# Optimization experiments

Measured on AMD Instinct MI355X. Metric: run time of the kernel, lower is better.

## Reference

```python
import jax, jax.numpy as jnp
import numpy as np

HEADS = 4
DIM_HEAD = 32
DIM = 128
EPS = 1e-5


def layer_norm(x, g, b):
    m = jnp.mean(x, axis=-1, keepdims=True)
    v = jnp.var(x, axis=-1, keepdims=True)
    return (x - m) * jax.lax.rsqrt(v + EPS) * g + b


def setup_inputs() -> dict:
    key = jax.random.key(0)
    ks = jax.random.split(key, 24)
    B, D, Hb, Wb = 1, DIM, 50, 50
    N, h, w = 6, 24, 44
    Q = Hb * Wb
    NK = N * h * w
    inner = HEADS * DIM_HEAD
    s = 0.02
    inp = {
        'q': jax.random.normal(ks[0], (B, D, Hb, Wb), jnp.float32),
        'k': jax.random.normal(ks[1], (B, N, D, h, w), jnp.float32),
        'v': jax.random.normal(ks[2], (B, N, D, h, w), jnp.float32),
        'W_logits': jax.random.uniform(ks[3], (B, Q, NK), jnp.float32),
        'vis': jax.random.randint(ks[4], (B, Q, NK), 0, 2, jnp.int32),
        'skip': jax.random.normal(ks[5], (B, D, Hb, Wb), jnp.float32),
        'qn_g': jnp.ones((D,)), 'qn_b': jnp.zeros((D,)),
        'kn_g': jnp.ones((D,)), 'kn_b': jnp.zeros((D,)),
        'vn_g': jnp.ones((D,)), 'vn_b': jnp.zeros((D,)),
        'wq': s * jax.random.normal(ks[6], (inner, D)), 'bq': jnp.zeros((inner,)),
        'wk': s * jax.random.normal(ks[7], (inner, D)), 'bk': jnp.zeros((inner,)),
        'wv': s * jax.random.normal(ks[8], (inner, D)), 'bv': jnp.zeros((inner,)),
        'wproj': s * jax.random.normal(ks[9], (D, inner)), 'bproj': jnp.zeros((D,)),
        'pre_g': jnp.ones((D,)), 'pre_b': jnp.zeros((D,)),
        'w1': s * jax.random.normal(ks[10], (2 * D, D)), 'b1': jnp.zeros((2 * D,)),
        'w2': s * jax.random.normal(ks[11], (D, 2 * D)), 'b2': jnp.zeros((D,)),
        'post_g': jnp.ones((D,)), 'post_b': jnp.zeros((D,)),
    }
    return inp


def reference(q, k, v, W_logits, vis, skip,
              qn_g, qn_b, kn_g, kn_b, vn_g, vn_b,
              wq, bq, wk, bk, wv, bv, wproj, bproj,
              pre_g, pre_b, w1, b1, w2, b2, post_g, post_b):
    B, D, Hb, Wb = q.shape
    Q = Hb * Wb
    scale = DIM_HEAD ** (-0.5)
    # flatten: q -> [B, Q, D]; k,v [B,N,D,h,w] -> [B, NK, D]
    qf = q.reshape(B, D, Q).transpose(0, 2, 1)
    kf = jnp.transpose(k, (0, 1, 3, 4, 2)).reshape(B, -1, D)
    vf = jnp.transpose(v, (0, 1, 3, 4, 2)).reshape(B, -1, D)
    qf = layer_norm(qf, qn_g, qn_b) @ wq.T + bq
    kf = layer_norm(kf, kn_g, kn_b) @ wk.T + bk
    vf = layer_norm(vf, vn_g, vn_b) @ wv.T + bv
    # split heads -> [B, H, Q/K, dh]
    qh = qf.reshape(B, Q, HEADS, DIM_HEAD).transpose(0, 2, 1, 3)
    kh = kf.reshape(B, -1, HEADS, DIM_HEAD).transpose(0, 2, 1, 3)
    vh = vf.reshape(B, -1, HEADS, DIM_HEAD).transpose(0, 2, 1, 3)
    logits = jnp.einsum('bhqd,bhkd->bhqk', qh, kh) * scale
    neg_inf = jnp.finfo(logits.dtype).min
    logits = jnp.where(vis[:, None] == 0, neg_inf, logits)
    logits = logits * W_logits[:, None]
    attn = jax.nn.softmax(logits, axis=-1)
    out = jnp.einsum('bhqk,bhkd->bhqd', attn, vh)
    out = out.transpose(0, 2, 1, 3).reshape(B, Q, HEADS * DIM_HEAD)
    out = out @ wproj.T + bproj
    z = out.transpose(0, 2, 1).reshape(B, D, Hb, Wb) + skip
    zf = z.reshape(B, D, Q).transpose(0, 2, 1)
    zf = layer_norm(zf, pre_g, pre_b)
    hmid = jax.nn.gelu(zf @ w1.T + b1, approximate=False)
    zf = zf + (hmid @ w2.T + b2)
    zf = layer_norm(zf, post_g, post_b)
    return zf.transpose(0, 2, 1).reshape(B, D, Hb, Wb)
```

## Files before the change

### kernel.cpp

```cpp
#include <hip/hip_runtime.h>
#include <hip/hip_bf16.h>

typedef __attribute__((ext_vector_type(8))) short bf16x8;
typedef __attribute__((ext_vector_type(4))) float f32x4;

#define NQ 2500
#define NKK 6336
#define NHEADS 4
#define DHEAD 32
#define CSC 0.25503482f
#define BIGNEG (-1.0e30f)

#define WS_QP 0
#define WS_KP 640000
#define WS_VT 2262016
#define WS_WB 3884032
#define WS_OP 4146176
#define OSPLIT_F 340000
#define OROW_F 136
#define WS_REQ3 8226176ULL
#define WS_REQ4 9586176ULL
#define WS_REQ6 12306176ULL

#define WQB 0
#define WKB 16384
#define WVB 32768
#define WPROJB 49152
#define W1B 65536
#define W2B 98304

#define NTILES_TOTAL 99
#define TQ 16
#define TK 64
#define QBLOCKS 157
#define MQBLOCKS 313

#define KSTR 136
#define VSTR 72
#define PSTR 72
#define ABSTR 68

__device__ __forceinline__ unsigned short bf16bits(float x) {
  union { __hip_bfloat16 h; unsigned short s; } cv;
  cv.h = __float2bfloat16(x);
  return cv.s;
}

__global__ __launch_bounds__(256) void wconv_kernel(
    const float* __restrict__ wq, const float* __restrict__ wk,
    const float* __restrict__ wv, const float* __restrict__ wproj,
    const float* __restrict__ w1, const float* __restrict__ w2,
    __hip_bfloat16* __restrict__ wb)
{
  int e = (blockIdx.x * 256 + threadIdx.x) * 4;
  const float* src; int off;
  if (e < 16384)      { src = wq;    off = e; }
  else if (e < 32768) { src = wk;    off = e - 16384; }
  else if (e < 49152) { src = wv;    off = e - 32768; }
  else if (e < 65536) { src = wproj; off = e - 49152; }
  else if (e < 98304) { src = w1;    off = e - 65536; }
  else                { src = w2;    off = e - 98304; }
  float4 v = *(const float4*)(src + off);
  ushort4 o4;
  o4.x = bf16bits(v.x); o4.y = bf16bits(v.y); o4.z = bf16bits(v.z); o4.w = bf16bits(v.w);
  *(ushort4*)((unsigned short*)wb + e) = o4;
}

__global__ __launch_bounds__(256) void lnproj_kernel(
    const float* __restrict__ qin, const float* __restrict__ kin, const float* __restrict__ vin,
    const float* __restrict__ qn_g, const float* __restrict__ qn_b,
    const float* __restrict__ kn_g, const float* __restrict__ kn_b,
    const float* __restrict__ vn_g, const float* __restrict__ vn_b,
    const __hip_bfloat16* __restrict__ wball,
    const float* __restrict__ bq, const float* __restrict__ bk, const float* __restrict__ bv,
    __hip_bfloat16* __restrict__ Qp, __hip_bfloat16* __restrict__ Kp,
    __hip_bfloat16* __restrict__ Vt)
{
  __shared__ __hip_bfloat16 lxb[32][136];
  __shared__ float lpart[32][8][2];
  __shared__ float lmr[32][2];
  __shared__ float lgb[128], lbeb[128];

  const int t = threadIdx.x;
  const int bb = blockIdx.x;
  int mode, row0;
  const float *in, *g, *be, *bo;
  const __hip_bfloat16* wb;
  if (bb < 79)       { mode = 0; row0 = bb * 32;         in = qin; g = qn_g; be = qn_b; wb = wball + WQB; bo = bq; }
  else if (bb < 277) { mode = 1; row0 = (bb - 79) * 32;  in = kin; g = kn_g; be = kn_b; wb = wball + WKB; bo = bk; }
  else               { mode = 2; row0 = (bb - 277) * 32; in = vin; g = vn_g; be = vn_b; wb = wball + WVB; bo = bv; }

  if (t < 128) { lgb[t] = g[t]; lbeb[t] = be[t]; }

  const int row = t & 31, seg = t >> 5;
  int grow = row0 + row;
  size_t base, dstr;
  bool rvalid = true;
  if (mode == 0) { rvalid = (grow < NQ); base = (size_t)(rvalid ? grow : NQ - 1); dstr = NQ; }
  else { int n = grow / 1056, rr = grow - n * 1056; base = (size_t)n * 135168 + rr; dstr = 1056; }

  float xr[16];
  float s = 0.f, ss = 0.f;
  #pragma unroll
  for (int i = 0; i < 16; ++i) {
    float x = in[base + (size_t)(seg * 16 + i) * dstr];
    xr[i] = x; s += x; ss += x * x;
  }
  lpart[row][seg][0] = s; lpart[row][seg][1] = ss;
  __syncthreads();
  if (t < 32) {
    float S = 0.f, SS = 0.f;
    #pragma unroll
    for (int j = 0; j < 8; ++j) { S += lpart[t][j][0]; SS += lpart[t][j][1]; }
    float mean = S * (1.f / 128.f);
    float var  = SS * (1.f / 128.f) - mean * mean;
    lmr[t][0] = mean;
    lmr[t][1] = rsqrtf(fmaxf(var, 0.f) + 1e-5f);
  }
  __syncthreads();
  {
    float mean = lmr[row][0], rstd = lmr[row][1];
    #pragma unroll
    for (int i = 0; i < 16; ++i) {
      int d = seg * 16 + i;
      lxb[row][d] = __float2bfloat16((xr[i] - mean) * rstd * lgb[d] + lbeb[d]);
    }
  }
  __syncthreads();

  const int wid = t >> 6, lane = t & 63;
  const int n16 = lane & 15, quad = lane >> 4;
  const int ow = wid * 32;

  f32x4 acc[2][2] = {};
  for (int kt = 0; kt < 4; ++kt) {
    bf16x8 af[2];
    #pragma unroll
    for (int mi = 0; mi < 2; ++mi)
      af[mi] = *(const bf16x8*)&lxb[mi * 16 + n16][kt * 32 + quad * 8];
    #pragma unroll
    for (int ni = 0; ni < 2; ++ni) {
      bf16x8 bw = *(const bf16x8*)(wb + (size_t)(ow + ni * 16 + n16) * 128 + kt * 32 + quad * 8);
      #pragma unroll
      for (int mi = 0; mi < 2; ++mi)
        acc[mi][ni] = __builtin_amdgcn_mfma_f32_16x16x32_bf16(af[mi], bw, acc[mi][ni], 0, 0, 0);
    }
  }

  float bias[2];
  #pragma unroll
  for (int ni = 0; ni < 2; ++ni) bias[ni] = bo[ow + ni * 16 + n16];

  #pragma unroll
  for (int mi = 0; mi < 2; ++mi) {
    int gr0 = row0 + mi * 16 + quad * 4;
    if (mode == 2) {
      #pragma unroll
      for (int ni = 0; ni < 2; ++ni) {
        int o = ow + ni * 16 + n16;
        ushort4 v4;
        v4.x = bf16bits(acc[mi][ni][0] + bias[ni]);
        v4.y = bf16bits(acc[mi][ni][1] + bias[ni]);
        v4.z = bf16bits(acc[mi][ni][2] + bias[ni]);
        v4.w = bf16bits(acc[mi][ni][3] + bias[ni]);
        *(ushort4*)((unsigned short*)Vt + (size_t)o * NKK + gr0) = v4;
      }
    } else {
      #pragma unroll
      for (int rg = 0; rg < 4; ++rg) {
        int gr = gr0 + rg;
        if (mode != 0 || gr < NQ) {
          #pragma unroll
          for (int ni = 0; ni < 2; ++ni) {
            int o = ow + ni * 16 + n16;
            __hip_bfloat16 b16 = __float2bfloat16(acc[mi][ni][rg] + bias[ni]);
            if (mode == 0) Qp[(size_t)gr * 128 + o] = b16;
            else           Kp[(size_t)gr * 128 + o] = b16;
          }
        }
      }
    }
  }
}

__global__ __launch_bounds__(256, 3) void attn_kernel(
    const __hip_bfloat16* __restrict__ Qp,
    const __hip_bfloat16* __restrict__ Kp,
    const __hip_bfloat16* __restrict__ Vt,
    const float* __restrict__ Wl,
    const int* __restrict__ vis,
    float* __restrict__ Opart)
{
  __shared__ alignas(16) __hip_bfloat16 lk[TK * KSTR];
  __shared__ alignas(16) __hip_bfloat16 lv[128 * VSTR];
  __shared__ alignas(16) float sc[TQ * ABSTR];
  __shared__ alignas(16) __hip_bfloat16 lp[NHEADS * TQ * PSTR];

  const int t = threadIdx.x;
  const int lane = t & 63;
  const int h = t >> 6;
  const int n16 = lane & 15;
  const int quad = lane >> 4;
  const int q0 = blockIdx.x * TQ;
  const int split = blockIdx.y;
  const int ksplit = gridDim.y;
  const int tstart = (NTILES_TOTAL * split) / ksplit;
  const int ntiles = (NTILES_TOTAL * (split + 1)) / ksplit - tstart;

  int gqa = q0 + n16; if (gqa >= NQ) gqa = NQ - 1;
  bf16x8 aq = *(const bf16x8*)(Qp + (size_t)gqa * 128 + h * DHEAD + quad * 8);

  const int kr = t >> 2, kc = (t & 3) * 32;
  const int vr = t >> 1, vc = (t & 1) * 32;
  const int e4 = t * 4, qq = e4 >> 6, kkc = e4 & 63;
  int gqe = q0 + qq; if (gqe >= NQ) gqe = NQ - 1;
  const size_t wbase = (size_t)gqe * NKK + kkc;

  bf16x8 bones;
  {
    short one = (short)0x3F80;
    short val = (n16 == 0) ? one : (short)0;
    #pragma unroll
    for (int j = 0; j < 8; ++j) bones[j] = val;
  }

  uint4 pk0, pk1, pk2, pk3, pv0, pv1, pv2, pv3;
  float4 pw; int4 pvs;

  auto issue = [&](int tile) {
    int k0 = (tstart + tile) * TK;
    const uint4* ksrc = (const uint4*)(Kp + (size_t)(k0 + kr) * 128 + kc);
    pk0 = ksrc[0]; pk1 = ksrc[1]; pk2 = ksrc[2]; pk3 = ksrc[3];
    const uint4* vsrc = (const uint4*)(Vt + (size_t)vr * NKK + k0 + vc);
    pv0 = vsrc[0]; pv1 = vsrc[1]; pv2 = vsrc[2]; pv3 = vsrc[3];
    pw  = *(const float4*)(Wl + wbase + k0);
    pvs = *(const int4*)(vis + wbase + k0);
  };
  auto commit = [&]() {
    uint4* kd = (uint4*)&lk[kr * KSTR + kc];
    kd[0] = pk0; kd[1] = pk1; kd[2] = pk2; kd[3] = pk3;
    uint4* vd = (uint4*)&lv[vr * VSTR + vc];
    vd[0] = pv0; vd[1] = pv1; vd[2] = pv2; vd[3] = pv3;
    float4 c4;
    c4.x = pvs.x ? pw.x * CSC : BIGNEG * pw.x;
    c4.y = pvs.y ? pw.y * CSC : BIGNEG * pw.y;
    c4.z = pvs.z ? pw.z * CSC : BIGNEG * pw.z;
    c4.w = pvs.w ? pw.w * CSC : BIGNEG * pw.w;
    *(float4*)&sc[qq * ABSTR + kkc] = c4;
  };

  f32x4 o0 = {0.f, 0.f, 0.f, 0.f};
  f32x4 o1 = {0.f, 0.f, 0.f, 0.f};
  f32x4 o2 = {0.f, 0.f, 0.f, 0.f};

  issue(0);
  commit();
  __syncthreads();

  for (int kt = 0; kt < ntiles; ++kt) {
    if (kt + 1 < ntiles) issue(kt + 1);

    f32x4 s[4];
    #pragma unroll
    for (int ks = 0; ks < 4; ++ks) {
      bf16x8 bk = *(const bf16x8*)&lk[(ks * 16 + n16) * KSTR + h * DHEAD + quad * 8];
      f32x4 z = {0.f, 0.f, 0.f, 0.f};
      s[ks] = __builtin_amdgcn_mfma_f32_16x16x32_bf16(aq, bk, z, 0, 0, 0);
    }
    #pragma unroll
    for (int ks = 0; ks < 4; ++ks) {
      #pragma unroll
      for (int r = 0; r < 4; ++r) {
        float c = sc[(quad * 4 + r) * ABSTR + ks * 16 + n16];
        float tt = s[ks][r] * c;
        float arg = (c >= 0.f) ? tt : c;
        float p = exp2f(fminf(arg, 60.f));
        lp[h * (TQ * PSTR) + (quad * 4 + r) * PSTR + ks * 16 + n16] = __float2bfloat16(p);
      }
    }
    #pragma unroll
    for (int kk = 0; kk < 2; ++kk) {
      bf16x8 ap  = *(const bf16x8*)&lp[h * (TQ * PSTR) + n16 * PSTR + kk * 32 + quad * 8];
      bf16x8 bv0 = *(const bf16x8*)&lv[(h * DHEAD + n16) * VSTR + kk * 32 + quad * 8];
      bf16x8 bv1 = *(const bf16x8*)&lv[(h * DHEAD + 16 + n16) * VSTR + kk * 32 + quad * 8];
      o0 = __builtin_amdgcn_mfma_f32_16x16x32_bf16(ap, bv0, o0, 0, 0, 0);
      o1 = __builtin_amdgcn_mfma_f32_16x16x32_bf16(ap, bv1, o1, 0, 0, 0);
      o2 = __builtin_amdgcn_mfma_f32_16x16x32_bf16(ap, bones, o2, 0, 0, 0);
    }

    if (kt + 1 < ntiles) {
      __syncthreads();
      commit();
      __syncthreads();
    }
  }

  #pragma unroll
  for (int r = 0; r < 4; ++r) {
    int gq = q0 + quad * 4 + r;
    if (gq < NQ) {
      float* rowp = Opart + (size_t)split * OSPLIT_F + (size_t)gq * OROW_F;
      rowp[h * DHEAD + n16] = o0[r];
      rowp[h * DHEAD + 16 + n16] = o1[r];
      if (n16 == 0) rowp[128 + h] = o2[r];
    }
  }
}

__global__ __launch_bounds__(256) void mlp_kernel(
    const float* __restrict__ Opart, int ksplit,
    const float* __restrict__ skip,
    const __hip_bfloat16* __restrict__ wball,
    const float* __restrict__ bproj,
    const float* __restrict__ pre_g, const float* __restrict__ pre_b,
    const float* __restrict__ b1, const float* __restrict__ b2,
    const float* __restrict__ post_g, const float* __restrict__ post_b,
    float* __restrict__ out)
{
  __shared__ __hip_bfloat16 sab[16][136];
  __shared__ __hip_bfloat16 znb[16][136];
  __shared__ float znf[16][132];
  __shared__ __hip_bfloat16 hb[16][264];
  __shared__ float part[16][4][2];

  const __hip_bfloat16* wprojb = wball + WPROJB;
  const __hip_bfloat16* w1b    = wball + W1B;
  const __hip_bfloat16* w2b    = wball + W2B;

  const int t = threadIdx.x;
  const int q0 = blockIdx.x * 8;

  {
    int row = t >> 4, c0 = (t & 15) * 8;
    int gq = q0 + row; int cq = gq < NQ ? gq : NQ - 1;
    int head = c0 >> 5;
    float ll = 0.f;
    float acc8[8] = {};
    for (int s = 0; s < ksplit; ++s) {
      const float* rp = Opart + (size_t)s * OSPLIT_F + (size_t)cq * OROW_F;
      ll += rp[128 + head];
      float4 a = *(const float4*)(rp + c0);
      float4 b = *(const float4*)(rp + c0 + 4);
      acc8[0] += a.x; acc8[1] += a.y; acc8[2] += a.z; acc8[3] += a.w;
      acc8[4] += b.x; acc8[5] += b.y; acc8[6] += b.z; acc8[7] += b.w;
    }
    float rll = 1.f / fmaxf(ll, 1e-30f);
    #pragma unroll
    for (int i = 0; i < 8; ++i)
      sab[row][c0 + i] = __float2bfloat16(acc8[i] * rll);
  }
  __syncthreads();

  const int wid = t >> 6, lane = t & 63;
  const int n16 = lane & 15, quad = lane >> 4;
  const int qrow0 = q0 + quad * 4;

  f32x4 acc1[2] = {};
  for (int kt = 0; kt < 4; ++kt) {
    bf16x8 af = *(const bf16x8*)&sab[n16][kt * 32 + quad * 8];
    #pragma unroll
    for (int ni = 0; ni < 2; ++ni) {
      int o = wid * 32 + ni * 16 + n16;
      bf16x8 bw = *(const bf16x8*)(wprojb + (size_t)o * 128 + kt * 32 + quad * 8);
      acc1[ni] = __builtin_amdgcn_mfma_f32_16x16x32_bf16(af, bw, acc1[ni], 0, 0, 0);
    }
  }
  float z[2][4];
  #pragma unroll
  for (int ni = 0; ni < 2; ++ni) {
    int o = wid * 32 + ni * 16 + n16;
    float bo = bproj[o];
    if (qrow0 + 3 < NQ) {
      float4 sk = *(const float4*)(skip + (size_t)o * NQ + qrow0);
      z[ni][0] = acc1[ni][0] + bo + sk.x;
      z[ni][1] = acc1[ni][1] + bo + sk.y;
      z[ni][2] = acc1[ni][2] + bo + sk.z;
      z[ni][3] = acc1[ni][3] + bo + sk.w;
    } else {
      #pragma unroll
      for (int rg = 0; rg < 4; ++rg) {
        int cq = qrow0 + rg < NQ ? qrow0 + rg : NQ - 1;
        z[ni][rg] = acc1[ni][rg] + bo + skip[(size_t)o * NQ + cq];
      }
    }
  }
  #pragma unroll
  for (int rg = 0; rg < 4; ++rg) {
    float s = z[0][rg] + z[1][rg];
    float ss = z[0][rg] * z[0][rg] + z[1][rg] * z[1][rg];
    s += __shfl_xor(s, 1);  ss += __shfl_xor(ss, 1);
    s += __shfl_xor(s, 2);  ss += __shfl_xor(ss, 2);
    s += __shfl_xor(s, 4);  ss += __shfl_xor(ss, 4);
    s += __shfl_xor(s, 8);  ss += __shfl_xor(ss, 8);
    if (n16 == 0) { part[quad * 4 + rg][wid][0] = s; part[quad * 4 + rg][wid][1] = ss; }
  }
  __syncthreads();
  #pragma unroll
  for (int rg = 0; rg < 4; ++rg) {
    int row = quad * 4 + rg;
    float S  = part[row][0][0] + part[row][1][0] + part[row][2][0] + part[row][3][0];
    float SS = part[row][0][1] + part[row][1][1] + part[row][2][1] + part[row][3][1];
    float mean = S * (1.f / 128.f);
    float var  = SS * (1.f / 128.f) - mean * mean;
    float rstd = rsqrtf(fmaxf(var, 0.f) + 1e-5f);
    #pragma unroll
    for (int ni = 0; ni < 2; ++ni) {
      int o = wid * 32 + ni * 16 + n16;
      float zn = (z[ni][rg] - mean) * rstd * pre_g[o] + pre_b[o];
      znf[row][o] = zn;
      znb[row][o] = __float2bfloat16(zn);
    }
  }
  __syncthreads();

  f32x4 acc2[4] = {};
  for (int kt = 0; kt < 4; ++kt) {
    bf16x8 af = *(const bf16x8*)&znb[n16][kt * 32 + quad * 8];
    #pragma unroll
    for (int ni = 0; ni < 4; ++ni) {
      int j = wid * 64 + ni * 16 + n16;
      bf16x8 bw = *(const bf16x8*)(w1b + (size_t)j * 128 + kt * 32 + quad * 8);
      acc2[ni] = __builtin_amdgcn_mfma_f32_16x16x32_bf16(af, bw, acc2[ni], 0, 0, 0);
    }
  }
  #pragma unroll
  for (int ni = 0; ni < 4; ++ni) {
    int j = wid * 64 + ni * 16 + n16;
    float bj = b1[j];
    #pragma unroll
    for (int rg = 0; rg < 4; ++rg) {
      float a1 = acc2[ni][rg] + bj;
      hb[quad * 4 + rg][j] = __float2bfloat16(0.5f * a1 * (1.0f + erff(a1 * 0.70710678118654752f)));
    }
  }
  __syncthreads();

  f32x4 acc3[2] = {};
  for (int kt = 0; kt < 8; ++kt) {
    bf16x8 af = *(const bf16x8*)&hb[n16][kt * 32 + quad * 8];
    #pragma unroll
    for (int ni = 0; ni < 2; ++ni) {
      int o = wid * 32 + ni * 16 + n16;
      bf16x8 bw = *(const bf16x8*)(w2b + (size_t)o * 256 + kt * 32 + quad * 8);
      acc3[ni] = __builtin_amdgcn_mfma_f32_16x16x32_bf16(af, bw, acc3[ni], 0, 0, 0);
    }
  }
  float y[2][4];
  #pragma unroll
  for (int ni = 0; ni < 2; ++ni) {
    int o = wid * 32 + ni * 16 + n16;
    float bo = b2[o];
    #pragma unroll
    for (int rg = 0; rg < 4; ++rg)
      y[ni][rg] = znf[quad * 4 + rg][o] + acc3[ni][rg] + bo;
  }
  #pragma unroll
  for (int rg = 0; rg < 4; ++rg) {
    float s = y[0][rg] + y[1][rg];
    float ss = y[0][rg] * y[0][rg] + y[1][rg] * y[1][rg];
    s += __shfl_xor(s, 1);  ss += __shfl_xor(ss, 1);
    s += __shfl_xor(s, 2);  ss += __shfl_xor(ss, 2);
    s += __shfl_xor(s, 4);  ss += __shfl_xor(ss, 4);
    s += __shfl_xor(s, 8);  ss += __shfl_xor(ss, 8);
    if (n16 == 0) { part[quad * 4 + rg][wid][0] = s; part[quad * 4 + rg][wid][1] = ss; }
  }
  __syncthreads();
  #pragma unroll
  for (int rg = 0; rg < 4; ++rg) {
    int row = quad * 4 + rg;
    float S  = part[row][0][0] + part[row][1][0] + part[row][2][0] + part[row][3][0];
    float SS = part[row][0][1] + part[row][1][1] + part[row][2][1] + part[row][3][1];
    float mean = S * (1.f / 128.f);
    float var  = SS * (1.f / 128.f) - mean * mean;
    float rstd = rsqrtf(fmaxf(var, 0.f) + 1e-5f);
    #pragma unroll
    for (int ni = 0; ni < 2; ++ni) {
      int o = wid * 32 + ni * 16 + n16;
      y[ni][rg] = (y[ni][rg] - mean) * rstd * post_g[o] + post_b[o];
    }
  }
  if (quad < 2) {
    #pragma unroll
    for (int ni = 0; ni < 2; ++ni) {
      int o = wid * 32 + ni * 16 + n16;
      if (qrow0 + 3 < NQ) {
        *(float4*)(out + (size_t)o * NQ + qrow0) = make_float4(y[ni][0], y[ni][1], y[ni][2], y[ni][3]);
      } else {
        #pragma unroll
        for (int rg = 0; rg < 4; ++rg)
          if (qrow0 + rg < NQ) out[(size_t)o * NQ + qrow0 + rg] = y[ni][rg];
      }
    }
  }
}

extern "C" void kernel_launch(void* const* d_in, const int* in_sizes, int n_in,
                              void* d_out, int out_size, void* d_ws, size_t ws_size,
                              hipStream_t stream) {
  if (ws_size < WS_REQ3) return;
  const int ksplit = (ws_size >= WS_REQ6) ? 6 : (ws_size >= WS_REQ4) ? 4 : 3;

  const float* q     = (const float*)d_in[0];
  const float* k     = (const float*)d_in[1];
  const float* v     = (const float*)d_in[2];
  const float* Wl    = (const float*)d_in[3];
  const int*   vis   = (const int*)d_in[4];
  const float* skip  = (const float*)d_in[5];
  const float* qn_g  = (const float*)d_in[6];
  const float* qn_b  = (const float*)d_in[7];
  const float* kn_g  = (const float*)d_in[8];
  const float* kn_b  = (const float*)d_in[9];
  const float* vn_g  = (const float*)d_in[10];
  const float* vn_b  = (const float*)d_in[11];
  const float* wq    = (const float*)d_in[12];
  const float* bq    = (const float*)d_in[13];
  const float* wk    = (const float*)d_in[14];
  const float* bk    = (const float*)d_in[15];
  const float* wv    = (const float*)d_in[16];
  const float* bv    = (const float*)d_in[17];
  const float* wproj = (const float*)d_in[18];
  const float* bproj = (const float*)d_in[19];
  const float* pre_g = (const float*)d_in[20];
  const float* pre_b = (const float*)d_in[21];
  const float* w1    = (const float*)d_in[22];
  const float* b1    = (const float*)d_in[23];
  const float* w2    = (const float*)d_in[24];
  const float* b2    = (const float*)d_in[25];
  const float* post_g= (const float*)d_in[26];
  const float* post_b= (const float*)d_in[27];

  char* ws = (char*)d_ws;
  __hip_bfloat16* Qp = (__hip_bfloat16*)(ws + WS_QP);
  __hip_bfloat16* Kp = (__hip_bfloat16*)(ws + WS_KP);
  __hip_bfloat16* Vt = (__hip_bfloat16*)(ws + WS_VT);
  __hip_bfloat16* Wb = (__hip_bfloat16*)(ws + WS_WB);
  float* Opart = (float*)(ws + WS_OP);

  hipLaunchKernelGGL(wconv_kernel, dim3(128), dim3(256), 0, stream,
                     wq, wk, wv, wproj, w1, w2, Wb);

  hipLaunchKernelGGL(lnproj_kernel, dim3(475), dim3(256), 0, stream,
                     q, k, v, qn_g, qn_b, kn_g, kn_b, vn_g, vn_b,
                     Wb, bq, bk, bv, Qp, Kp, Vt);

  hipLaunchKernelGGL(attn_kernel, dim3(QBLOCKS, ksplit), dim3(256), 0, stream,
                     Qp, Kp, Vt, Wl, vis, Opart);

  hipLaunchKernelGGL(mlp_kernel, dim3(MQBLOCKS), dim3(256), 0, stream,
                     Opart, ksplit, skip, Wb, bproj, pre_g, pre_b,
                     b1, b2, post_g, post_b, (float*)d_out);
}
```

Measured before the change: 273.3 us.

## Double attention query tile to 32 rows and widen MLP blocks to 16 queries

The attention kernel now processes 32 query rows per block (two 16-row MFMA tiles) so every K/V tile staged in LDS is reused across twice as many queries, halving the K/V global traffic and staging per query. Launch bounds drop from 3 to 2 blocks per CU and the grid shrinks to 79 q-blocks. The mask/weight staging moves to 8 elements per thread. The MLP kernel now handles 16 queries per block with all quads writing output, so it launches half as many blocks. The costs are more registers and LDS per block and fewer blocks to spread across CUs.

```diff
diff --git a/kernel.cpp b/kernel.cpp
--- a/kernel.cpp
+++ b/kernel.cpp
@@ -31,9 +31,10 @@
 
 #define NTILES_TOTAL 99
 #define TQ 16
+#define ATQ 32
 #define TK 64
 #define QBLOCKS 157
-#define MQBLOCKS 313
+#define AQBLOCKS 79
 
 #define KSTR 136
 #define VSTR 72
@@ -183,7 +184,7 @@
   }
 }
 
-__global__ __launch_bounds__(256, 3) void attn_kernel(
+__global__ __launch_bounds__(256, 2) void attn_kernel(
     const __hip_bfloat16* __restrict__ Qp,
     const __hip_bfloat16* __restrict__ Kp,
     const __hip_bfloat16* __restrict__ Vt,
@@ -193,26 +194,30 @@
 {
   __shared__ alignas(16) __hip_bfloat16 lk[TK * KSTR];
   __shared__ alignas(16) __hip_bfloat16 lv[128 * VSTR];
-  __shared__ alignas(16) float sc[TQ * ABSTR];
-  __shared__ alignas(16) __hip_bfloat16 lp[NHEADS * TQ * PSTR];
+  __shared__ alignas(16) float sc[ATQ * ABSTR];
+  __shared__ alignas(16) __hip_bfloat16 lp[NHEADS * ATQ * PSTR];
 
   const int t = threadIdx.x;
   const int lane = t & 63;
   const int h = t >> 6;
   const int n16 = lane & 15;
   const int quad = lane >> 4;
-  const int q0 = blockIdx.x * TQ;
+  const int q0 = blockIdx.x * ATQ;
   const int split = blockIdx.y;
   const int ksplit = gridDim.y;
   const int tstart = (NTILES_TOTAL * split) / ksplit;
   const int ntiles = (NTILES_TOTAL * (split + 1)) / ksplit - tstart;
 
-  int gqa = q0 + n16; if (gqa >= NQ) gqa = NQ - 1;
-  bf16x8 aq = *(const bf16x8*)(Qp + (size_t)gqa * 128 + h * DHEAD + quad * 8);
+  bf16x8 aq[2];
+  #pragma unroll
+  for (int m = 0; m < 2; ++m) {
+    int gqa = q0 + m * 16 + n16; if (gqa >= NQ) gqa = NQ - 1;
+    aq[m] = *(const bf16x8*)(Qp + (size_t)gqa * 128 + h * DHEAD + quad * 8);
+  }
 
   const int kr = t >> 2, kc = (t & 3) * 32;
   const int vr = t >> 1, vc = (t & 1) * 32;
-  const int e4 = t * 4, qq = e4 >> 6, kkc = e4 & 63;
+  const int qq = t >> 3, kkc = (t & 7) * 8;
   int gqe = q0 + qq; if (gqe >= NQ) gqe = NQ - 1;
   const size_t wbase = (size_t)gqe * NKK + kkc;
 
@@ -225,7 +230,7 @@
   }
 
   uint4 pk0, pk1, pk2, pk3, pv0, pv1, pv2, pv3;
-  float4 pw; int4 pvs;
+  float4 pw0, pw1; int4 pvs0, pvs1;
 
   auto issue = [&](int tile) {
     int k0 = (tstart + tile) * TK;
@@ -233,25 +238,35 @@
     pk0 = ksrc[0]; pk1 = ksrc[1]; pk2 = ksrc[2]; pk3 = ksrc[3];
     const uint4* vsrc = (const uint4*)(Vt + (size_t)vr * NKK + k0 + vc);
     pv0 = vsrc[0]; pv1 = vsrc[1]; pv2 = vsrc[2]; pv3 = vsrc[3];
-    pw  = *(const float4*)(Wl + wbase + k0);
-    pvs = *(const int4*)(vis + wbase + k0);
+    pw0  = *(const float4*)(Wl + wbase + k0);
+    pw1  = *(const float4*)(Wl + wbase + k0 + 4);
+    pvs0 = *(const int4*)(vis + wbase + k0);
+    pvs1 = *(const int4*)(vis + wbase + k0 + 4);
   };
   auto commit = [&]() {
     uint4* kd = (uint4*)&lk[kr * KSTR + kc];
     kd[0] = pk0; kd[1] = pk1; kd[2] = pk2; kd[3] = pk3;
     uint4* vd = (uint4*)&lv[vr * VSTR + vc];
     vd[0] = pv0; vd[1] = pv1; vd[2] = pv2; vd[3] = pv3;
-    float4 c4;
-    c4.x = pvs.x ? pw.x * CSC : BIGNEG * pw.x;
-    c4.y = pvs.y ? pw.y * CSC : BIGNEG * pw.y;
-    c4.z = pvs.z ? pw.z * CSC : BIGNEG * pw.z;
-    c4.w = pvs.w ? pw.w * CSC : BIGNEG * pw.w;
-    *(float4*)&sc[qq * ABSTR + kkc] = c4;
+    float4 c0, c1;
+    c0.x = pvs0.x ? pw0.x * CSC : BIGNEG * pw0.x;
+    c0.y = pvs0.y ? pw0.y * CSC : BIGNEG * pw0.y;
+    c0.z = pvs0.z ? pw0.z * CSC : BIGNEG * pw0.z;
+    c0.w = pvs0.w ? pw0.w * CSC : BIGNEG * pw0.w;
+    c1.x = pvs1.x ? pw1.x * CSC : BIGNEG * pw1.x;
+    c1.y = pvs1.y ? pw1.y * CSC : BIGNEG * pw1.y;
+    c1.z = pvs1.z ? pw1.z * CSC : BIGNEG * pw1.z;
+    c1.w = pvs1.w ? pw1.w * CSC : BIGNEG * pw1.w;
+    *(float4*)&sc[qq * ABSTR + kkc] = c0;
+    *(float4*)&sc[qq * ABSTR + kkc + 4] = c1;
   };
 
-  f32x4 o0 = {0.f, 0.f, 0.f, 0.f};
-  f32x4 o1 = {0.f, 0.f, 0.f, 0.f};
-  f32x4 o2 = {0.f, 0.f, 0.f, 0.f};
+  f32x4 o[2][3];
+  #pragma unroll
+  for (int m = 0; m < 2; ++m)
+    #pragma unroll
+    for (int j = 0; j < 3; ++j)
+      o[m][j] = f32x4{0.f, 0.f, 0.f, 0.f};
 
   issue(0);
   commit();
@@ -260,32 +275,40 @@
   for (int kt = 0; kt < ntiles; ++kt) {
     if (kt + 1 < ntiles) issue(kt + 1);
 
-    f32x4 s[4];
+    f32x4 s[2][4];
     #pragma unroll
     for (int ks = 0; ks < 4; ++ks) {
       bf16x8 bk = *(const bf16x8*)&lk[(ks * 16 + n16) * KSTR + h * DHEAD + quad * 8];
       f32x4 z = {0.f, 0.f, 0.f, 0.f};
-      s[ks] = __builtin_amdgcn_mfma_f32_16x16x32_bf16(aq, bk, z, 0, 0, 0);
-    }
-    #pragma unroll
-    for (int ks = 0; ks < 4; ++ks) {
-      #pragma unroll
-      for (int r = 0; r < 4; ++r) {
-        float c = sc[(quad * 4 + r) * ABSTR + ks * 16 + n16];
-        float tt = s[ks][r] * c;
-        float arg = (c >= 0.f) ? tt : c;
-        float p = exp2f(fminf(arg, 60.f));
-        lp[h * (TQ * PSTR) + (quad * 4 + r) * PSTR + ks * 16 + n16] = __float2bfloat16(p);
+      s[0][ks] = __builtin_amdgcn_mfma_f32_16x16x32_bf16(aq[0], bk, z, 0, 0, 0);
+      s[1][ks] = __builtin_amdgcn_mfma_f32_16x16x32_bf16(aq[1], bk, z, 0, 0, 0);
+    }
+    #pragma unroll
+    for (int m = 0; m < 2; ++m) {
+      #pragma unroll
+      for (int ks = 0; ks < 4; ++ks) {
+        #pragma unroll
+        for (int r = 0; r < 4; ++r) {
+          int row = m * 16 + quad * 4 + r;
+          float c = sc[row * ABSTR + ks * 16 + n16];
+          float tt = s[m][ks][r] * c;
+          float arg = (c >= 0.f) ? tt : c;
+          float p = exp2f(fminf(arg, 60.f));
+          lp[h * (ATQ * PSTR) + row * PSTR + ks * 16 + n16] = __float2bfloat16(p);
+        }
       }
     }
     #pragma unroll
     for (int kk = 0; kk < 2; ++kk) {
-      bf16x8 ap  = *(const bf16x8*)&lp[h * (TQ * PSTR) + n16 * PSTR + kk * 32 + quad * 8];
       bf16x8 bv0 = *(const bf16x8*)&lv[(h * DHEAD + n16) * VSTR + kk * 32 + quad * 8];
       bf16x8 bv1 = *(const bf16x8*)&lv[(h * DHEAD + 16 + n16) * VSTR + kk * 32 + quad * 8];
-      o0 = __builtin_amdgcn_mfma_f32_16x16x32_bf16(ap, bv0, o0, 0, 0, 0);
-      o1 = __builtin_amdgcn_mfma_f32_16x16x32_bf16(ap, bv1, o1, 0, 0, 0);
-      o2 = __builtin_amdgcn_mfma_f32_16x16x32_bf16(ap, bones, o2, 0, 0, 0);
+      #pragma unroll
+      for (int m = 0; m < 2; ++m) {
+        bf16x8 ap = *(const bf16x8*)&lp[h * (ATQ * PSTR) + (m * 16 + n16) * PSTR + kk * 32 + quad * 8];
+        o[m][0] = __builtin_amdgcn_mfma_f32_16x16x32_bf16(ap, bv0, o[m][0], 0, 0, 0);
+        o[m][1] = __builtin_amdgcn_mfma_f32_16x16x32_bf16(ap, bv1, o[m][1], 0, 0, 0);
+        o[m][2] = __builtin_amdgcn_mfma_f32_16x16x32_bf16(ap, bones, o[m][2], 0, 0, 0);
+      }
     }
 
     if (kt + 1 < ntiles) {
@@ -296,13 +319,16 @@
   }
 
   #pragma unroll
-  for (int r = 0; r < 4; ++r) {
-    int gq = q0 + quad * 4 + r;
-    if (gq < NQ) {
-      float* rowp = Opart + (size_t)split * OSPLIT_F + (size_t)gq * OROW_F;
-      rowp[h * DHEAD + n16] = o0[r];
-      rowp[h * DHEAD + 16 + n16] = o1[r];
-      if (n16 == 0) rowp[128 + h] = o2[r];
+  for (int m = 0; m < 2; ++m) {
+    #pragma unroll
+    for (int r = 0; r < 4; ++r) {
+      int gq = q0 + m * 16 + quad * 4 + r;
+      if (gq < NQ) {
+        float* rowp = Opart + (size_t)split * OSPLIT_F + (size_t)gq * OROW_F;
+        rowp[h * DHEAD + n16] = o[m][0][r];
+        rowp[h * DHEAD + 16 + n16] = o[m][1][r];
+        if (n16 == 0) rowp[128 + h] = o[m][2][r];
+      }
     }
   }
 }
@@ -328,7 +354,7 @@
   const __hip_bfloat16* w2b    = wball + W2B;
 
   const int t = threadIdx.x;
-  const int q0 = blockIdx.x * 8;
+  const int q0 = blockIdx.x * TQ;
 
   {
     int row = t >> 4, c0 = (t & 15) * 8;
@@ -479,17 +505,15 @@
       y[ni][rg] = (y[ni][rg] - mean) * rstd * post_g[o] + post_b[o];
     }
   }
-  if (quad < 2) {
-    #pragma unroll
-    for (int ni = 0; ni < 2; ++ni) {
-      int o = wid * 32 + ni * 16 + n16;
-      if (qrow0 + 3 < NQ) {
-        *(float4*)(out + (size_t)o * NQ + qrow0) = make_float4(y[ni][0], y[ni][1], y[ni][2], y[ni][3]);
-      } else {
-        #pragma unroll
-        for (int rg = 0; rg < 4; ++rg)
-          if (qrow0 + rg < NQ) out[(size_t)o * NQ + qrow0 + rg] = y[ni][rg];
-      }
+  #pragma unroll
+  for (int ni = 0; ni < 2; ++ni) {
+    int o = wid * 32 + ni * 16 + n16;
+    if (qrow0 + 3 < NQ) {
+      *(float4*)(out + (size_t)o * NQ + qrow0) = make_float4(y[ni][0], y[ni][1], y[ni][2], y[ni][3]);
+    } else {
+      #pragma unroll
+      for (int rg = 0; rg < 4; ++rg)
+        if (qrow0 + rg < NQ) out[(size_t)o * NQ + qrow0 + rg] = y[ni][rg];
     }
   }
 }
@@ -543,10 +567,10 @@
                      q, k, v, qn_g, qn_b, kn_g, kn_b, vn_g, vn_b,
                      Wb, bq, bk, bv, Qp, Kp, Vt);
 
-  hipLaunchKernelGGL(attn_kernel, dim3(QBLOCKS, ksplit), dim3(256), 0, stream,
+  hipLaunchKernelGGL(attn_kernel, dim3(AQBLOCKS, ksplit), dim3(256), 0, stream,
                      Qp, Kp, Vt, Wl, vis, Opart);
 
-  hipLaunchKernelGGL(mlp_kernel, dim3(MQBLOCKS), dim3(256), 0, stream,
+  hipLaunchKernelGGL(mlp_kernel, dim3(QBLOCKS), dim3(256), 0, stream,
                      Opart, ksplit, skip, Wb, bproj, pre_g, pre_b,
                      b1, b2, post_g, post_b, (float*)d_out);
 }
```

After: 249.2 us. -8.8%, faster.
